# Kernel tuning notes

Measured on AMD Instinct MI355X. Metric: run time of the kernel, lower is better.

The kernel has to match this reference:

```python
import jax, jax.numpy as jnp
import numpy as np

B, T, DIM = 2, 1024, 1024
H, DH, E, K = 8, 64, 5, 3
SCALE = DH ** -0.5


def topk_mask(scores, k):
    # 0/1 mask of the top-k entries along the last (expert) axis
    _, idx = jax.lax.top_k(scores, k)          # [..., k]
    return jax.nn.one_hot(idx, scores.shape[-1], dtype=scores.dtype).sum(-2)


def setup_inputs() -> dict:
    key = jax.random.key(0)
    ks = jax.random.split(key, 7)
    s = DIM ** -0.5
    x = jax.random.normal(ks[0], (B, T, DIM), jnp.float32)
    Wq = jax.random.normal(ks[1], (DIM, H * DH), jnp.float32) * s
    Wk = jax.random.normal(ks[2], (DIM, H * DH), jnp.float32) * s
    Wv = jax.random.normal(ks[3], (DIM, H * E * DH), jnp.float32) * s
    Ws = jax.random.normal(ks[4], (DIM, H * E), jnp.float32) * s
    Wd = jax.random.normal(ks[5], (DIM, H * E), jnp.float32) * s
    # grouped conv weight: per head h, expert e: map dim_head -> dim
    Wo = jax.random.normal(ks[6], (H, E, DIM, DH), jnp.float32) * (DH ** -0.5)
    causal_mask = jnp.triu(jnp.ones((T, T), bool), 1)[None, None]  # [1,1,T,T]
    return {"x": x, "Wq": Wq, "Wk": Wk, "Wv": Wv, "Ws": Ws, "Wd": Wd,
            "Wo": Wo, "causal_mask": causal_mask}


def reference(x, Wq, Wk, Wv, Ws, Wd, Wo, causal_mask):
    # source-side routing scores (soft: gate values kept on top-k)
    ss = jax.nn.sigmoid((x @ Ws).reshape(B, T, H, E))
    ss = ss * topk_mask(ss, K)
    # destination-side routing (hard 0/1 top-k mask)
    sd = topk_mask(jax.nn.sigmoid((x @ Wd).reshape(B, T, H, E)), K)

    q = (x @ Wq).reshape(B, T, H, DH).transpose(0, 2, 1, 3)  # [B,H,T,DH]
    k = (x @ Wk).reshape(B, T, H, DH).transpose(0, 2, 1, 3)
    v_exp = (x @ Wv).reshape(B, T, H, E, DH)                  # per-expert V
    v = jnp.einsum('bthe,bthed->bhtd', ss, v_exp)             # routed V mix

    scores = jnp.einsum('bhid,bhjd->bhij', q * SCALE, k)
    scores = jnp.where(causal_mask, -1e9, scores)
    probs = jax.nn.softmax(scores, axis=-1)
    o = jnp.einsum('bhij,bhjd->bhid', probs, v)               # [B,H,T,DH]

    # expert output projection (h,e: DH -> DIM), gated by sd, summed over h,e
    out = jnp.einsum('bthe,bhtc,hedc->btd', sd, o, Wo)        # [B,T,DIM]
    return out
```

## Files before the change

### kernel.cpp

```cpp
#include <hip/hip_runtime.h>

typedef unsigned short u16;
typedef unsigned long long u64;
typedef __bf16 bf16x8 __attribute__((ext_vector_type(8)));
typedef float floatx4 __attribute__((ext_vector_type(4)));

#define B_   2
#define T_   1024
#define DIM_ 1024
#define H_   8
#define DH_  64
#define E_   5

#define N1   3584
#define M_   2048
#define KOUT 2560

__device__ __forceinline__ u16 f2bf(float f) {
  union { float f; unsigned u; } v; v.f = f;
  unsigned r = v.u + 0x7FFFu + ((v.u >> 16) & 1u);
  return (u16)(r >> 16);
}
__device__ __forceinline__ float bf2f(u16 h) {
  union { unsigned u; float f; } v; v.u = ((unsigned)h) << 16;
  return v.f;
}

__device__ __forceinline__ void async_cp16(const void* g, void* l) {
  __builtin_amdgcn_global_load_lds(
      (const __attribute__((address_space(1))) unsigned int*)g,
      (__attribute__((address_space(3))) unsigned int*)l, 16, 0, 0);
}


__global__ __launch_bounds__(256)
void prep_kernel(const float* __restrict__ Wq, const float* __restrict__ Wk,
                 const float* __restrict__ Wv, const float* __restrict__ Wo,
                 u16* __restrict__ WT, u16* __restrict__ WoT) {
  __shared__ float tile[32][33];
  if (blockIdx.y < 112) {
    int k0 = blockIdx.x * 32;
    int nt = blockIdx.y;
    const float* W; int N, n0, nofs;
    if (nt < 16)      { W = Wq; N = 512;  n0 = nt * 32;        nofs = 0; }
    else if (nt < 32) { W = Wk; N = 512;  n0 = (nt - 16) * 32; nofs = 512; }
    else              { W = Wv; N = 2560; n0 = (nt - 32) * 32; nofs = 1024; }
    int tx = threadIdx.x & 31, ty = threadIdx.x >> 5;
    #pragma unroll
    for (int i = 0; i < 32; i += 8)
      tile[ty + i][tx] = W[(size_t)(k0 + ty + i) * N + n0 + tx];
    __syncthreads();
    #pragma unroll
    for (int i = 0; i < 32; i += 8)
      WT[(size_t)(nofs + n0 + ty + i) * 1024 + k0 + tx] = f2bf(tile[tx][ty + i]);
  } else {
    int id = (blockIdx.y - 112) * 32 + blockIdx.x;
    int i = id * 256 + threadIdx.x;
    int c4 = i & 15;
    int t  = i >> 4;
    int d  = t / 40;
    int he = t - d * 40;
    float4 v = *(const float4*)(Wo + ((size_t)(he * 1024 + d) * 64 + c4 * 4));
    union { u16 s[4]; uint2 u; } o;
    o.s[0] = f2bf(v.x); o.s[1] = f2bf(v.y); o.s[2] = f2bf(v.z); o.s[3] = f2bf(v.w);
    *(uint2*)(WoT + (size_t)d * KOUT + he * 64 + c4 * 4) = o.u;
  }
}


__global__ __launch_bounds__(256)
void logits_kernel(const float* __restrict__ x, const float* __restrict__ Ws,
                   const float* __restrict__ Wd, float* __restrict__ Pl,
                   u16* __restrict__ xb) {
  __shared__ float xs[16][68];
  __shared__ float wt[16][80];
  const int tid = threadIdx.x;
  const int m0 = blockIdx.x * 64;
  const int kbeg = blockIdx.y * 128;
  const int tx = tid & 15, ty = tid >> 4;
  const int srow = tid >> 2, skq = tid & 3;

  float acc[4][5];
  #pragma unroll
  for (int r = 0; r < 4; ++r)
    #pragma unroll
    for (int c = 0; c < 5; ++c) acc[r][c] = 0.f;

  for (int s = 0; s < 8; ++s) {
    const int k0 = kbeg + s * 16;
    __syncthreads();
    {
      float4 v = *(const float4*)(x + (size_t)(m0 + srow) * 1024 + k0 + skq * 4);
      xs[skq * 4 + 0][srow] = v.x; xs[skq * 4 + 1][srow] = v.y;
      xs[skq * 4 + 2][srow] = v.z; xs[skq * 4 + 3][srow] = v.w;
      union { u16 h[4]; uint2 u; } o;
      o.h[0] = f2bf(v.x); o.h[1] = f2bf(v.y); o.h[2] = f2bf(v.z); o.h[3] = f2bf(v.w);
      *(uint2*)(xb + (size_t)(m0 + srow) * 1024 + k0 + skq * 4) = o.u;
    }
    #pragma unroll
    for (int j = 0; j < 5; ++j) {
      int f = j * 256 + tid;
      int kk = f / 80, c = f - kk * 80;
      wt[kk][c] = (c < 40) ? Ws[(size_t)(k0 + kk) * 40 + c]
                           : Wd[(size_t)(k0 + kk) * 40 + c - 40];
    }
    __syncthreads();

    #pragma unroll
    for (int kk = 0; kk < 16; ++kk) {
      float4 xv = *(const float4*)(&xs[kk][ty * 4]);
      float xr[4] = {xv.x, xv.y, xv.z, xv.w};
      #pragma unroll
      for (int c = 0; c < 5; ++c) {
        float wv = wt[kk][tx * 5 + c];
        #pragma unroll
        for (int r = 0; r < 4; ++r) acc[r][c] = fmaf(xr[r], wv, acc[r][c]);
      }
    }
  }

  float* P = Pl + (size_t)blockIdx.y * M_ * 80;
  #pragma unroll
  for (int r = 0; r < 4; ++r)
    #pragma unroll
    for (int c = 0; c < 5; ++c)
      P[(size_t)(m0 + ty * 4 + r) * 80 + tx * 5 + c] = acc[r][c];
}

__global__ __launch_bounds__(256)
void topk_kernel(const float* __restrict__ Pl, float* __restrict__ ssg,
                 u64* __restrict__ sdb) {
  __shared__ float lg[16][80];
  __shared__ unsigned char mb[16][8];
  const int bt0 = blockIdx.x * 16;
  const int tid = threadIdx.x;
  #pragma unroll
  for (int j = 0; j < 5; ++j) {
    int f = j * 256 + tid;
    int r = f / 80, c = f - r * 80;
    float s = 0.f;
    #pragma unroll
    for (int z = 0; z < 8; ++z)
      s += Pl[(size_t)z * M_ * 80 + (size_t)(bt0 + r) * 80 + c];
    lg[r][c] = s;
  }
  __syncthreads();

  const int r = tid >> 4, h = (tid >> 1) & 7, side = tid & 1;
  float z[E_], g[E_]; bool sel[E_];
  #pragma unroll
  for (int e = 0; e < E_; ++e) {
    z[e] = lg[r][side * 40 + h * E_ + e];
    g[e] = 1.f / (1.f + __expf(-z[e]));
    sel[e] = false;
  }
  #pragma unroll
  for (int it = 0; it < 3; ++it) {
    int bi = 0; float bv = -3e38f;
    #pragma unroll
    for (int e = 0; e < E_; ++e)
      if (!sel[e] && z[e] > bv) { bv = z[e]; bi = e; }
    sel[bi] = true;
  }
  if (side == 0) {
    #pragma unroll
    for (int e = 0; e < E_; ++e)
      ssg[(size_t)(bt0 + r) * 40 + h * E_ + e] = sel[e] ? g[e] : 0.f;
  } else {
    unsigned bits = 0;
    #pragma unroll
    for (int e = 0; e < E_; ++e) bits |= (sel[e] ? 1u : 0u) << e;
    mb[r][h] = (unsigned char)bits;
  }
  __syncthreads();
  if (tid < 16) {
    u64 m = 0;
    #pragma unroll
    for (int hh = 0; hh < 8; ++hh) m |= (u64)mb[tid][hh] << (5 * hh);
    sdb[bt0 + tid] = m;
  }
}


__global__ __launch_bounds__(256)
void gemm4w_kernel(const u16* __restrict__ A, const u16* __restrict__ Bm,
                   u16* __restrict__ C, int N, int Kd) {
  constexpr int BK = 32;
  __shared__ __align__(16) u16 As[128 * BK];
  __shared__ __align__(16) u16 Bs[128 * BK];
  const int tid = threadIdx.x;
  const int w = tid >> 6, lane = tid & 63;
  const int ln15 = lane & 15, quad = lane >> 4;
  const int wm = w >> 1, wn = w & 1;
  const int bm0 = blockIdx.x * 128, bn0 = blockIdx.y * 128;
  const int lrow = lane >> 2;
  const int lg8 = (((lane & 3) ^ ((lane >> 3) & 3))) * 8;
  const int swz = (ln15 >> 1) & 3;

  floatx4 acc[4][4];
  #pragma unroll
  for (int i = 0; i < 4; ++i)
    #pragma unroll
    for (int j = 0; j < 4; ++j) acc[i][j] = (floatx4){0.f, 0.f, 0.f, 0.f};

  for (int k0 = 0; k0 < Kd; k0 += BK) {
    __syncthreads();
    #pragma unroll
    for (int j = 0; j < 2; ++j) {
      int i = w * 2 + j;
      async_cp16(A + (size_t)(bm0 + i * 16 + lrow) * Kd + k0 + lg8, (char*)As + i * 1024);
      async_cp16(Bm + (size_t)(bn0 + i * 16 + lrow) * Kd + k0 + lg8, (char*)Bs + i * 1024);
    }
    __builtin_amdgcn_s_waitcnt(0);
    __syncthreads();

    bf16x8 af[4], bf[4];
    #pragma unroll
    for (int mt = 0; mt < 4; ++mt)
      af[mt] = *(const bf16x8*)(As + (wm * 64 + mt * 16 + ln15) * BK + ((quad ^ swz) * 8));
    #pragma unroll
    for (int nt = 0; nt < 4; ++nt)
      bf[nt] = *(const bf16x8*)(Bs + (wn * 64 + nt * 16 + ln15) * BK + ((quad ^ swz) * 8));
    #pragma unroll
    for (int mt = 0; mt < 4; ++mt)
      #pragma unroll
      for (int nt = 0; nt < 4; ++nt)
        acc[mt][nt] = __builtin_amdgcn_mfma_f32_16x16x32_bf16(af[mt], bf[nt], acc[mt][nt], 0, 0, 0);
  }

  #pragma unroll
  for (int mt = 0; mt < 4; ++mt)
    #pragma unroll
    for (int nt = 0; nt < 4; ++nt)
      #pragma unroll
      for (int r = 0; r < 4; ++r) {
        int m = bm0 + wm * 64 + mt * 16 + quad * 4 + r;
        int n = bn0 + wn * 64 + nt * 16 + ln15;
        C[(size_t)m * N + n] = f2bf(acc[mt][nt][r]);
      }
}


__global__ __launch_bounds__(256)
void gemm2f_kernel(const u16* __restrict__ o_bh, const u16* __restrict__ WoT,
                   const u64* __restrict__ sdb, u16* __restrict__ Pk) {
  constexpr int BK = 32, Kd = KOUT;
  __shared__ __align__(16) u16 As[128 * BK];
  __shared__ __align__(16) u16 Bs[128 * BK];
  const int tid = threadIdx.x;
  const int w = tid >> 6, lane = tid & 63;
  const int ln15 = lane & 15, quad = lane >> 4;
  const int wm = w >> 1, wn = w & 1;
  const int bm0 = blockIdx.x * 128, bn0 = blockIdx.y * 128;
  const int b = bm0 >> 10;
  const int t_base = bm0 & 1023;
  const int lrow = lane >> 2;
  const int lg8 = (((lane & 3) ^ ((lane >> 3) & 3))) * 8;
  const int swz = (ln15 >> 1) & 3;
  const int kbeg = blockIdx.z * 640;

  u64 sdr[4];
  #pragma unroll
  for (int mt = 0; mt < 4; ++mt)
    sdr[mt] = sdb[bm0 + wm * 64 + mt * 16 + ln15];

  floatx4 acc[4][4];
  #pragma unroll
  for (int i = 0; i < 4; ++i)
    #pragma unroll
    for (int j = 0; j < 4; ++j) acc[i][j] = (floatx4){0.f, 0.f, 0.f, 0.f};

  for (int k0 = kbeg; k0 < kbeg + 640; k0 += BK) {
    const int he = k0 >> 6;
    const int h = (he * 205) >> 10;
    const int c0 = k0 & 63;
    const u16* abase = o_bh + ((size_t)((b * 8 + h) * 1024 + t_base) * 64) + c0;
    __syncthreads();
    #pragma unroll
    for (int j = 0; j < 2; ++j) {
      int i = w * 2 + j;
      async_cp16(abase + (size_t)(i * 16 + lrow) * 64 + lg8, (char*)As + i * 1024);
      async_cp16(WoT + (size_t)(bn0 + i * 16 + lrow) * Kd + k0 + lg8, (char*)Bs + i * 1024);
    }
    __builtin_amdgcn_s_waitcnt(0);
    __syncthreads();

    bf16x8 af[4], bf[4];
    union { uint4 u; bf16x8 v; } z8; z8.u = (uint4){0u, 0u, 0u, 0u};
    #pragma unroll
    for (int mt = 0; mt < 4; ++mt) {
      af[mt] = *(const bf16x8*)(As + (wm * 64 + mt * 16 + ln15) * BK + ((quad ^ swz) * 8));
      if (!((sdr[mt] >> he) & 1)) af[mt] = z8.v;
    }
    #pragma unroll
    for (int nt = 0; nt < 4; ++nt)
      bf[nt] = *(const bf16x8*)(Bs + (wn * 64 + nt * 16 + ln15) * BK + ((quad ^ swz) * 8));
    #pragma unroll
    for (int mt = 0; mt < 4; ++mt)
      #pragma unroll
      for (int nt = 0; nt < 4; ++nt)
        acc[mt][nt] = __builtin_amdgcn_mfma_f32_16x16x32_bf16(af[mt], bf[nt], acc[mt][nt], 0, 0, 0);
  }

  u16* Cz = Pk + (size_t)blockIdx.z * M_ * 1024;
  #pragma unroll
  for (int mt = 0; mt < 4; ++mt)
    #pragma unroll
    for (int nt = 0; nt < 4; ++nt)
      #pragma unroll
      for (int r = 0; r < 4; ++r) {
        int m = bm0 + wm * 64 + mt * 16 + quad * 4 + r;
        int n = bn0 + wn * 64 + nt * 16 + ln15;
        Cz[(size_t)m * 1024 + n] = f2bf(acc[mt][nt][r]);
      }
}

__global__ void reduce4_kernel(const u16* __restrict__ Pk, float* __restrict__ out) {
  int i = blockIdx.x * 256 + threadIdx.x;
  size_t base = (size_t)i * 8;
  float s[8] = {0.f, 0.f, 0.f, 0.f, 0.f, 0.f, 0.f, 0.f};
  #pragma unroll
  for (int z = 0; z < 4; ++z) {
    union { uint4 v; u16 h[8]; } u;
    u.v = *(const uint4*)(Pk + (size_t)z * M_ * 1024 + base);
    #pragma unroll
    for (int c = 0; c < 8; ++c) s[c] += bf2f(u.h[c]);
  }
  float4 o0 = {s[0], s[1], s[2], s[3]}, o1 = {s[4], s[5], s[6], s[7]};
  *(float4*)(out + base) = o0;
  *(float4*)(out + base + 4) = o1;
}


__global__ __launch_bounds__(256)
void vmix_tr_kernel(const u16* __restrict__ c1, const float* __restrict__ ssg,
                    u16* __restrict__ vT) {
  __shared__ u16 tile[32][33];
  const int bh = blockIdx.x;
  const int b = bh >> 3, h = bh & 7;
  const int t0 = blockIdx.y * 32, d0 = blockIdx.z * 32;
  const int dh = threadIdx.x & 31, tl = threadIdx.x >> 5;
  #pragma unroll
  for (int i = 0; i < 4; ++i) {
    int trow = tl + i * 8;
    size_t bt = (size_t)b * T_ + t0 + trow;
    const u16* ve = c1 + bt * N1 + 1024 + h * (E_ * 64) + d0 + dh;
    const float* g = ssg + bt * 40 + h * E_;
    float s = 0.f;
    #pragma unroll
    for (int e = 0; e < E_; ++e) s = fmaf(g[e], bf2f(ve[e * 64]), s);
    tile[trow][dh] = f2bf(s);
  }
  __syncthreads();
  #pragma unroll
  for (int i = 0; i < 4; ++i) {
    int d = d0 + tl + i * 8;
    vT[((size_t)(b * H_ + h) * DH_ + d) * T_ + t0 + dh] = tile[dh][tl + i * 8];
  }
}


__global__ __launch_bounds__(256)
void attn_kernel(const u16* __restrict__ c1, const u16* __restrict__ vT,
                 u16* __restrict__ o_bh) {
  __shared__ __align__(16) u16 Qs[32 * 64];
  __shared__ __align__(16) u16 Ks[2][64 * 64];
  __shared__ __align__(16) u16 Vs[2][64 * 64];
  __shared__ __align__(16) u16 Ps[2][32 * 72];
  __shared__ float Om[2][32][68];
  __shared__ float Ml[2][32], Ll[2][32];
  const int bx = blockIdx.x;
  const int qi = (bx & 1) ? (bx >> 1) : (31 - (bx >> 1));
  const int bh = blockIdx.y;
  const int b = bh >> 3, h = bh & 7;
  const int tid = threadIdx.x;
  const int w = tid >> 6, lane = tid & 63;
  const int ln15 = lane & 15, quad = lane >> 4;
  const int hh = w >> 1, wq = w & 1;
  const int q0 = qi * 32;
  const int nkt = (qi >> 1) + 1;
  const int h0n = (nkt + 1) >> 1;
  const int r8 = lane >> 3;
  const int g8 = ((lane & 7) ^ ((lane >> 3) & 7)) * 8;
  const int swz = ln15 & 7;

  async_cp16(c1 + (size_t)(b * T_ + q0 + w * 8 + r8) * N1 + h * DH_ + g8,
             (char*)Qs + w * 1024);

  floatx4 O[4];
  float m_st[4], l_st[4];
  #pragma unroll
  for (int j = 0; j < 4; ++j) {
    O[j] = (floatx4){0.f, 0.f, 0.f, 0.f};
    m_st[j] = -3e38f; l_st[j] = 0.f;
  }
  const int qrow = q0 + wq * 16 + quad * 4;

  for (int j = 0; j < h0n; ++j) {
    const int myt = hh ? (h0n + j) : j;
    const bool act = (hh == 0) || (h0n + j < nkt);
    __syncthreads();
    if (w < 2 || h0n + j < nkt) {
      const int tk = (w < 2 ? j : h0n + j) * 64;
      if ((w & 1) == 0) {
        #pragma unroll
        for (int i = 0; i < 8; ++i)
          async_cp16(c1 + (size_t)(b * T_ + tk + i * 8 + r8) * N1 + 512 + h * DH_ + g8,
                     (char*)Ks[w >> 1] + i * 1024);
      } else {
        #pragma unroll
        for (int i = 0; i < 8; ++i)
          async_cp16(vT + (size_t)((b * H_ + h) * DH_ + i * 8 + r8) * T_ + tk + g8,
                     (char*)Vs[w >> 1] + i * 1024);
      }
    }
    __builtin_amdgcn_s_waitcnt(0);
    __syncthreads();

    float p[4][4];
    if (act) {
      const int tk0 = myt * 64;
      floatx4 S[4];
      #pragma unroll
      for (int nt = 0; nt < 4; ++nt) S[nt] = (floatx4){0.f, 0.f, 0.f, 0.f};
      #pragma unroll
      for (int ks = 0; ks < 2; ++ks) {
        bf16x8 a = *(const bf16x8*)(Qs + (wq * 16 + ln15) * 64 + (((ks * 4 + quad) ^ swz)) * 8);
        #pragma unroll
        for (int nt = 0; nt < 4; ++nt) {
          bf16x8 bv = *(const bf16x8*)(&Ks[hh][(nt * 16 + ln15) * 64 + (((ks * 4 + quad) ^ swz)) * 8]);
          S[nt] = __builtin_amdgcn_mfma_f32_16x16x32_bf16(a, bv, S[nt], 0, 0, 0);
        }
      }
      float rmax[4], alpha[4], rsum[4];
      #pragma unroll
      for (int r = 0; r < 4; ++r) rmax[r] = -3e38f;
      #pragma unroll
      for (int nt = 0; nt < 4; ++nt) {
        int col = tk0 + nt * 16 + ln15;
        #pragma unroll
        for (int r = 0; r < 4; ++r) {
          float s = S[nt][r] * 0.125f;
          if (col > qrow + r) s = -3e38f;
          p[nt][r] = s;
          rmax[r] = fmaxf(rmax[r], s);
        }
      }
      #pragma unroll
      for (int r = 0; r < 4; ++r) {
        #pragma unroll
        for (int off = 1; off < 16; off <<= 1)
          rmax[r] = fmaxf(rmax[r], __shfl_xor(rmax[r], off));
        float mn = fmaxf(m_st[r], rmax[r]);
        alpha[r] = __expf(m_st[r] - mn);
        m_st[r] = mn;
        rsum[r] = 0.f;
      }
      #pragma unroll
      for (int nt = 0; nt < 4; ++nt)
        #pragma unroll
        for (int r = 0; r < 4; ++r) {
          float e = __expf(p[nt][r] - m_st[r]);
          p[nt][r] = e;
          rsum[r] += e;
        }
      #pragma unroll
      for (int r = 0; r < 4; ++r) {
        #pragma unroll
        for (int off = 1; off < 16; off <<= 1)
          rsum[r] += __shfl_xor(rsum[r], off);
        l_st[r] = l_st[r] * alpha[r] + rsum[r];
      }
      #pragma unroll
      for (int nt = 0; nt < 4; ++nt)
        #pragma unroll
        for (int r = 0; r < 4; ++r) O[nt][r] *= alpha[r];
      #pragma unroll
      for (int nt = 0; nt < 4; ++nt)
        #pragma unroll
        for (int r = 0; r < 4; ++r)
          Ps[hh][(wq * 16 + quad * 4 + r) * 72 + nt * 16 + ln15] = f2bf(p[nt][r]);
    }
    __syncthreads();
    if (act) {
      #pragma unroll
      for (int ks = 0; ks < 2; ++ks) {
        bf16x8 a = *(const bf16x8*)(&Ps[hh][(wq * 16 + ln15) * 72 + ks * 32 + quad * 8]);
        #pragma unroll
        for (int nt = 0; nt < 4; ++nt) {
          bf16x8 bv = *(const bf16x8*)(&Vs[hh][(nt * 16 + ln15) * 64 + (((ks * 4 + quad) ^ swz)) * 8]);
          O[nt] = __builtin_amdgcn_mfma_f32_16x16x32_bf16(a, bv, O[nt], 0, 0, 0);
        }
      }
    }
  }

  #pragma unroll
  for (int nt = 0; nt < 4; ++nt)
    #pragma unroll
    for (int r = 0; r < 4; ++r)
      Om[hh][wq * 16 + quad * 4 + r][nt * 16 + ln15] = O[nt][r];
  if (ln15 == 0) {
    #pragma unroll
    for (int r = 0; r < 4; ++r) {
      Ml[hh][wq * 16 + quad * 4 + r] = m_st[r];
      Ll[hh][wq * 16 + quad * 4 + r] = l_st[r];
    }
  }
  __syncthreads();

  const int rr = tid >> 3, cg = (tid & 7) * 8;
  float m0 = Ml[0][rr], m1 = Ml[1][rr];
  float l0 = Ll[0][rr], l1 = Ll[1][rr];
  float m = fmaxf(m0, m1);
  float a0 = __expf(m0 - m), a1 = __expf(m1 - m);
  float inv = 1.f / (l0 * a0 + l1 * a1);
  union { u16 s[8]; uint4 v; } o;
  #pragma unroll
  for (int cc = 0; cc < 8; ++cc)
    o.s[cc] = f2bf((Om[0][rr][cg + cc] * a0 + Om[1][rr][cg + cc] * a1) * inv);
  *(uint4*)(o_bh + ((size_t)((b * 8 + h) * 1024 + q0 + rr)) * 64 + cg) = o.v;
}


extern "C" void kernel_launch(void* const* d_in, const int* in_sizes, int n_in,
                              void* d_out, int out_size, void* d_ws, size_t ws_size,
                              hipStream_t stream) {
  const float* x  = (const float*)d_in[0];
  const float* Wq = (const float*)d_in[1];
  const float* Wk = (const float*)d_in[2];
  const float* Wv = (const float*)d_in[3];
  const float* Ws = (const float*)d_in[4];
  const float* Wd = (const float*)d_in[5];
  const float* Wo = (const float*)d_in[6];
  float* out = (float*)d_out;

  char* ws = (char*)d_ws;
  u16*   WoT  = (u16*)(ws + 0);
  u16*   xb   = (u16*)(ws + 5242880);
  u16*   WT   = (u16*)(ws + 9437184);
  u16*   c1   = (u16*)(ws + 16777216);
  float* ssg  = (float*)(ws + 31457280);
  u64*   sdb  = (u64*)(ws + 31784960);
  u16*   o_bh = (u16*)(ws + 31801344);
  u16*   vT   = (u16*)(ws + 33898496);
  u16*   Pk   = (u16*)(ws + 35995648);
  float* Pl   = (float*)(ws + 52772864);

  logits_kernel<<<dim3(32, 8), 256, 0, stream>>>(x, Ws, Wd, Pl, xb);
  topk_kernel<<<128, 256, 0, stream>>>(Pl, ssg, sdb);

  prep_kernel<<<dim3(32, 192), 256, 0, stream>>>(Wq, Wk, Wv, Wo, WT, WoT);

  gemm4w_kernel<<<dim3(16, 28), 256, 0, stream>>>(xb, WT, c1, N1, 1024);

  vmix_tr_kernel<<<dim3(16, 32, 2), 256, 0, stream>>>(c1, ssg, vT);

  attn_kernel<<<dim3(32, 16), 256, 0, stream>>>(c1, vT, o_bh);

  gemm2f_kernel<<<dim3(16, 8, 4), 256, 0, stream>>>(o_bh, WoT, sdb, Pk);
  reduce4_kernel<<<1024, 256, 0, stream>>>(Pk, out);
}
```

Before: 186.9 us.

## Fuse logits, top-k and weight prep into one preamble kernel; widen GEMM BK to 64

Merges the routing-logit GEMV, top-k selection and the weight transpose/convert passes into one launch. Each routing block computes full-K logits for 8 rows using shuffles and LDS reduction, so the partial-logit buffer and its extra kernel disappear. The two bf16 MFMA GEMMs now use a 64-wide K tile with an 8-way XOR swizzle and launch_bounds(256,2), halving the number of barrier/load rounds. In exchange the GEMMs use more LDS per block, and the routing blocks read Ws/Wd straight from global memory without staging them in LDS.

```diff
diff --git a/kernel.cpp b/kernel.cpp
--- a/kernel.cpp
+++ b/kernel.cpp
@@ -32,170 +32,171 @@
       (__attribute__((address_space(3))) unsigned int*)l, 16, 0, 0);
 }
 
+#define XI(r, k) ((r) * 1088 + (k) + (((k) >> 6) << 2))
 
 __global__ __launch_bounds__(256)
-void prep_kernel(const float* __restrict__ Wq, const float* __restrict__ Wk,
-                 const float* __restrict__ Wv, const float* __restrict__ Wo,
-                 u16* __restrict__ WT, u16* __restrict__ WoT) {
-  __shared__ float tile[32][33];
-  if (blockIdx.y < 112) {
-    int k0 = blockIdx.x * 32;
-    int nt = blockIdx.y;
-    const float* W; int N, n0, nofs;
-    if (nt < 16)      { W = Wq; N = 512;  n0 = nt * 32;        nofs = 0; }
-    else if (nt < 32) { W = Wk; N = 512;  n0 = (nt - 16) * 32; nofs = 512; }
-    else              { W = Wv; N = 2560; n0 = (nt - 32) * 32; nofs = 1024; }
-    int tx = threadIdx.x & 31, ty = threadIdx.x >> 5;
-    #pragma unroll
-    for (int i = 0; i < 32; i += 8)
-      tile[ty + i][tx] = W[(size_t)(k0 + ty + i) * N + n0 + tx];
-    __syncthreads();
-    #pragma unroll
-    for (int i = 0; i < 32; i += 8)
-      WT[(size_t)(nofs + n0 + ty + i) * 1024 + k0 + tx] = f2bf(tile[tx][ty + i]);
-  } else {
-    int id = (blockIdx.y - 112) * 32 + blockIdx.x;
-    int i = id * 256 + threadIdx.x;
-    int c4 = i & 15;
-    int t  = i >> 4;
-    int d  = t / 40;
-    int he = t - d * 40;
-    float4 v = *(const float4*)(Wo + ((size_t)(he * 1024 + d) * 64 + c4 * 4));
-    union { u16 s[4]; uint2 u; } o;
-    o.s[0] = f2bf(v.x); o.s[1] = f2bf(v.y); o.s[2] = f2bf(v.z); o.s[3] = f2bf(v.w);
-    *(uint2*)(WoT + (size_t)d * KOUT + he * 64 + c4 * 4) = o.u;
-  }
-}
-
-
-__global__ __launch_bounds__(256)
-void logits_kernel(const float* __restrict__ x, const float* __restrict__ Ws,
-                   const float* __restrict__ Wd, float* __restrict__ Pl,
-                   u16* __restrict__ xb) {
-  __shared__ float xs[16][68];
-  __shared__ float wt[16][80];
+void preamble_kernel(const float* __restrict__ x, const float* __restrict__ Wq,
+                     const float* __restrict__ Wk, const float* __restrict__ Wv,
+                     const float* __restrict__ Ws, const float* __restrict__ Wd,
+                     const float* __restrict__ Wo,
+                     u16* __restrict__ WT, u16* __restrict__ WoT,
+                     float* __restrict__ ssg, u64* __restrict__ sdb,
+                     u16* __restrict__ xb) {
+  __shared__ __align__(16) char smem[47744];
+  const int bx = blockIdx.x;
   const int tid = threadIdx.x;
-  const int m0 = blockIdx.x * 64;
-  const int kbeg = blockIdx.y * 128;
-  const int tx = tid & 15, ty = tid >> 4;
-  const int srow = tid >> 2, skq = tid & 3;
-
-  float acc[4][5];
-  #pragma unroll
-  for (int r = 0; r < 4; ++r)
+
+  if (bx >= 256) {
+    const int pb = bx - 256;
+    const int kx = pb & 31, nt = pb >> 5;
+    if (nt < 112) {
+      float (*tile)[33] = (float(*)[33])smem;
+      int k0 = kx * 32;
+      const float* W; int N, n0, nofs;
+      if (nt < 16)      { W = Wq; N = 512;  n0 = nt * 32;        nofs = 0; }
+      else if (nt < 32) { W = Wk; N = 512;  n0 = (nt - 16) * 32; nofs = 512; }
+      else              { W = Wv; N = 2560; n0 = (nt - 32) * 32; nofs = 1024; }
+      int tx = tid & 31, ty = tid >> 5;
+      #pragma unroll
+      for (int i = 0; i < 32; i += 8)
+        tile[ty + i][tx] = W[(size_t)(k0 + ty + i) * N + n0 + tx];
+      __syncthreads();
+      #pragma unroll
+      for (int i = 0; i < 32; i += 8)
+        WT[(size_t)(nofs + n0 + ty + i) * 1024 + k0 + tx] = f2bf(tile[tx][ty + i]);
+    } else {
+      int id = (nt - 112) * 32 + kx;
+      int i = id * 256 + tid;
+      int c4 = i & 15;
+      int t  = i >> 4;
+      int d  = t / 40;
+      int he = t - d * 40;
+      float4 v = *(const float4*)(Wo + ((size_t)(he * 1024 + d) * 64 + c4 * 4));
+      union { u16 s[4]; uint2 u; } o;
+      o.s[0] = f2bf(v.x); o.s[1] = f2bf(v.y); o.s[2] = f2bf(v.z); o.s[3] = f2bf(v.w);
+      *(uint2*)(WoT + (size_t)d * KOUT + he * 64 + c4 * 4) = o.u;
+    }
+    return;
+  }
+
+  float* xs = (float*)smem;
+  float* ps = xs + 8 * 1088;
+  float* lg = ps + 4 * 640;
+  unsigned char* mb = (unsigned char*)(lg + 640);
+  const int bt0 = bx * 8;
+
+  for (int i = tid; i < 2048; i += 256) {
+    int r = i >> 8, j = i & 255;
+    float4 v = ((const float4*)(x + (size_t)(bt0 + r) * 1024))[j];
+    *(float4*)(xs + XI(r, j * 4)) = v;
+    union { u16 h[4]; uint2 u; } o;
+    o.h[0] = f2bf(v.x); o.h[1] = f2bf(v.y); o.h[2] = f2bf(v.z); o.h[3] = f2bf(v.w);
+    *(uint2*)(xb + (size_t)(bt0 + r) * 1024 + j * 4) = o.u;
+  }
+  __syncthreads();
+
+  const int cx = tid & 15;
+  const int ky = tid >> 4;
+  float acc[8][5];
+  #pragma unroll
+  for (int r = 0; r < 8; ++r)
     #pragma unroll
     for (int c = 0; c < 5; ++c) acc[r][c] = 0.f;
 
-  for (int s = 0; s < 8; ++s) {
-    const int k0 = kbeg + s * 16;
-    __syncthreads();
-    {
-      float4 v = *(const float4*)(x + (size_t)(m0 + srow) * 1024 + k0 + skq * 4);
-      xs[skq * 4 + 0][srow] = v.x; xs[skq * 4 + 1][srow] = v.y;
-      xs[skq * 4 + 2][srow] = v.z; xs[skq * 4 + 3][srow] = v.w;
-      union { u16 h[4]; uint2 u; } o;
-      o.h[0] = f2bf(v.x); o.h[1] = f2bf(v.y); o.h[2] = f2bf(v.z); o.h[3] = f2bf(v.w);
-      *(uint2*)(xb + (size_t)(m0 + srow) * 1024 + k0 + skq * 4) = o.u;
-    }
-    #pragma unroll
-    for (int j = 0; j < 5; ++j) {
-      int f = j * 256 + tid;
-      int kk = f / 80, c = f - kk * 80;
-      wt[kk][c] = (c < 40) ? Ws[(size_t)(k0 + kk) * 40 + c]
-                           : Wd[(size_t)(k0 + kk) * 40 + c - 40];
-    }
-    __syncthreads();
-
-    #pragma unroll
-    for (int kk = 0; kk < 16; ++kk) {
-      float4 xv = *(const float4*)(&xs[kk][ty * 4]);
-      float xr[4] = {xv.x, xv.y, xv.z, xv.w};
-      #pragma unroll
-      for (int c = 0; c < 5; ++c) {
-        float wv = wt[kk][tx * 5 + c];
-        #pragma unroll
-        for (int r = 0; r < 4; ++r) acc[r][c] = fmaf(xr[r], wv, acc[r][c]);
-      }
-    }
-  }
-
-  float* P = Pl + (size_t)blockIdx.y * M_ * 80;
-  #pragma unroll
-  for (int r = 0; r < 4; ++r)
-    #pragma unroll
-    for (int c = 0; c < 5; ++c)
-      P[(size_t)(m0 + ty * 4 + r) * 80 + tx * 5 + c] = acc[r][c];
-}
-
-__global__ __launch_bounds__(256)
-void topk_kernel(const float* __restrict__ Pl, float* __restrict__ ssg,
-                 u64* __restrict__ sdb) {
-  __shared__ float lg[16][80];
-  __shared__ unsigned char mb[16][8];
-  const int bt0 = blockIdx.x * 16;
-  const int tid = threadIdx.x;
-  #pragma unroll
-  for (int j = 0; j < 5; ++j) {
-    int f = j * 256 + tid;
-    int r = f / 80, c = f - r * 80;
-    float s = 0.f;
-    #pragma unroll
-    for (int z = 0; z < 8; ++z)
-      s += Pl[(size_t)z * M_ * 80 + (size_t)(bt0 + r) * 80 + c];
-    lg[r][c] = s;
+  for (int q4 = 0; q4 < 16; ++q4) {
+    const int k = ky * 64 + q4 * 4;
+    float4 xr[8];
+    #pragma unroll
+    for (int r = 0; r < 8; ++r) xr[r] = *(const float4*)(xs + XI(r, k));
+    #pragma unroll
+    for (int c = 0; c < 5; ++c) {
+      const int col = cx * 5 + c;
+      const float* Wp = (col < 40) ? (Ws + col) : (Wd + col - 40);
+      float w0 = Wp[(size_t)(k + 0) * 40], w1 = Wp[(size_t)(k + 1) * 40];
+      float w2 = Wp[(size_t)(k + 2) * 40], w3 = Wp[(size_t)(k + 3) * 40];
+      #pragma unroll
+      for (int r = 0; r < 8; ++r) {
+        float a = acc[r][c];
+        a = fmaf(xr[r].x, w0, a); a = fmaf(xr[r].y, w1, a);
+        a = fmaf(xr[r].z, w2, a); a = fmaf(xr[r].w, w3, a);
+        acc[r][c] = a;
+      }
+    }
+  }
+
+  #pragma unroll
+  for (int r = 0; r < 8; ++r)
+    #pragma unroll
+    for (int c = 0; c < 5; ++c) {
+      float a = acc[r][c];
+      a += __shfl_xor(a, 16);
+      a += __shfl_xor(a, 32);
+      acc[r][c] = a;
+    }
+  const int w = tid >> 6, lane = tid & 63;
+  if (lane < 16) {
+    #pragma unroll
+    for (int r = 0; r < 8; ++r)
+      #pragma unroll
+      for (int c = 0; c < 5; ++c)
+        ps[w * 640 + r * 80 + lane * 5 + c] = acc[r][c];
   }
   __syncthreads();
-
-  const int r = tid >> 4, h = (tid >> 1) & 7, side = tid & 1;
-  float z[E_], g[E_]; bool sel[E_];
-  #pragma unroll
-  for (int e = 0; e < E_; ++e) {
-    z[e] = lg[r][side * 40 + h * E_ + e];
-    g[e] = 1.f / (1.f + __expf(-z[e]));
-    sel[e] = false;
-  }
-  #pragma unroll
-  for (int it = 0; it < 3; ++it) {
-    int bi = 0; float bv = -3e38f;
-    #pragma unroll
-    for (int e = 0; e < E_; ++e)
-      if (!sel[e] && z[e] > bv) { bv = z[e]; bi = e; }
-    sel[bi] = true;
-  }
-  if (side == 0) {
-    #pragma unroll
-    for (int e = 0; e < E_; ++e)
-      ssg[(size_t)(bt0 + r) * 40 + h * E_ + e] = sel[e] ? g[e] : 0.f;
-  } else {
-    unsigned bits = 0;
-    #pragma unroll
-    for (int e = 0; e < E_; ++e) bits |= (sel[e] ? 1u : 0u) << e;
-    mb[r][h] = (unsigned char)bits;
-  }
+  for (int idx = tid; idx < 640; idx += 256)
+    lg[idx] = ps[idx] + ps[640 + idx] + ps[1280 + idx] + ps[1920 + idx];
   __syncthreads();
-  if (tid < 16) {
+
+  if (tid < 128) {
+    const int r = tid >> 4, h = (tid >> 1) & 7, side = tid & 1;
+    float z[E_], g[E_]; bool sel[E_];
+    #pragma unroll
+    for (int e = 0; e < E_; ++e) {
+      z[e] = lg[r * 80 + side * 40 + h * E_ + e];
+      g[e] = 1.f / (1.f + __expf(-z[e]));
+      sel[e] = false;
+    }
+    #pragma unroll
+    for (int it = 0; it < 3; ++it) {
+      int bi = 0; float bv = -3e38f;
+      #pragma unroll
+      for (int e = 0; e < E_; ++e)
+        if (!sel[e] && z[e] > bv) { bv = z[e]; bi = e; }
+      sel[bi] = true;
+    }
+    if (side == 0) {
+      #pragma unroll
+      for (int e = 0; e < E_; ++e)
+        ssg[(size_t)(bt0 + r) * 40 + h * E_ + e] = sel[e] ? g[e] : 0.f;
+    } else {
+      unsigned bits = 0;
+      #pragma unroll
+      for (int e = 0; e < E_; ++e) bits |= (sel[e] ? 1u : 0u) << e;
+      mb[r * 8 + h] = (unsigned char)bits;
+    }
+  }
+  __syncthreads();
+  if (tid < 8) {
     u64 m = 0;
     #pragma unroll
-    for (int hh = 0; hh < 8; ++hh) m |= (u64)mb[tid][hh] << (5 * hh);
+    for (int hh = 0; hh < 8; ++hh) m |= (u64)mb[tid * 8 + hh] << (5 * hh);
     sdb[bt0 + tid] = m;
   }
 }
 
 
-__global__ __launch_bounds__(256)
+__global__ __launch_bounds__(256, 2)
 void gemm4w_kernel(const u16* __restrict__ A, const u16* __restrict__ Bm,
                    u16* __restrict__ C, int N, int Kd) {
-  constexpr int BK = 32;
-  __shared__ __align__(16) u16 As[128 * BK];
-  __shared__ __align__(16) u16 Bs[128 * BK];
+  __shared__ __align__(16) u16 As[128 * 64];
+  __shared__ __align__(16) u16 Bs[128 * 64];
   const int tid = threadIdx.x;
   const int w = tid >> 6, lane = tid & 63;
   const int ln15 = lane & 15, quad = lane >> 4;
   const int wm = w >> 1, wn = w & 1;
   const int bm0 = blockIdx.x * 128, bn0 = blockIdx.y * 128;
-  const int lrow = lane >> 2;
-  const int lg8 = (((lane & 3) ^ ((lane >> 3) & 3))) * 8;
-  const int swz = (ln15 >> 1) & 3;
+  const int r8 = lane >> 3;
+  const int g8 = ((lane & 7) ^ r8) * 8;
+  const int swz = ln15 & 7;
 
   floatx4 acc[4][4];
   #pragma unroll
@@ -203,29 +204,32 @@
     #pragma unroll
     for (int j = 0; j < 4; ++j) acc[i][j] = (floatx4){0.f, 0.f, 0.f, 0.f};
 
-  for (int k0 = 0; k0 < Kd; k0 += BK) {
-    __syncthreads();
-    #pragma unroll
-    for (int j = 0; j < 2; ++j) {
-      int i = w * 2 + j;
-      async_cp16(A + (size_t)(bm0 + i * 16 + lrow) * Kd + k0 + lg8, (char*)As + i * 1024);
-      async_cp16(Bm + (size_t)(bn0 + i * 16 + lrow) * Kd + k0 + lg8, (char*)Bs + i * 1024);
+  for (int k0 = 0; k0 < Kd; k0 += 64) {
+    __syncthreads();
+    #pragma unroll
+    for (int j = 0; j < 4; ++j) {
+      int i = w * 4 + j;
+      async_cp16(A + (size_t)(bm0 + i * 8 + r8) * Kd + k0 + g8, (char*)As + i * 1024);
+      async_cp16(Bm + (size_t)(bn0 + i * 8 + r8) * Kd + k0 + g8, (char*)Bs + i * 1024);
     }
     __builtin_amdgcn_s_waitcnt(0);
     __syncthreads();
 
-    bf16x8 af[4], bf[4];
-    #pragma unroll
-    for (int mt = 0; mt < 4; ++mt)
-      af[mt] = *(const bf16x8*)(As + (wm * 64 + mt * 16 + ln15) * BK + ((quad ^ swz) * 8));
-    #pragma unroll
-    for (int nt = 0; nt < 4; ++nt)
-      bf[nt] = *(const bf16x8*)(Bs + (wn * 64 + nt * 16 + ln15) * BK + ((quad ^ swz) * 8));
-    #pragma unroll
-    for (int mt = 0; mt < 4; ++mt)
+    #pragma unroll
+    for (int t = 0; t < 2; ++t) {
+      bf16x8 af[4], bf[4];
+      #pragma unroll
+      for (int mt = 0; mt < 4; ++mt)
+        af[mt] = *(const bf16x8*)(As + (wm * 64 + mt * 16 + ln15) * 64 + (((t * 4 + quad) ^ swz) * 8));
       #pragma unroll
       for (int nt = 0; nt < 4; ++nt)
-        acc[mt][nt] = __builtin_amdgcn_mfma_f32_16x16x32_bf16(af[mt], bf[nt], acc[mt][nt], 0, 0, 0);
+        bf[nt] = *(const bf16x8*)(Bs + (wn * 64 + nt * 16 + ln15) * 64 + (((t * 4 + quad) ^ swz) * 8));
+      #pragma unroll
+      for (int mt = 0; mt < 4; ++mt)
+        #pragma unroll
+        for (int nt = 0; nt < 4; ++nt)
+          acc[mt][nt] = __builtin_amdgcn_mfma_f32_16x16x32_bf16(af[mt], bf[nt], acc[mt][nt], 0, 0, 0);
+    }
   }
 
   #pragma unroll
@@ -241,12 +245,11 @@
 }
 
 
-__global__ __launch_bounds__(256)
+__global__ __launch_bounds__(256, 2)
 void gemm2f_kernel(const u16* __restrict__ o_bh, const u16* __restrict__ WoT,
                    const u64* __restrict__ sdb, u16* __restrict__ Pk) {
-  constexpr int BK = 32, Kd = KOUT;
-  __shared__ __align__(16) u16 As[128 * BK];
-  __shared__ __align__(16) u16 Bs[128 * BK];
+  __shared__ __align__(16) u16 As[128 * 64];
+  __shared__ __align__(16) u16 Bs[128 * 64];
   const int tid = threadIdx.x;
   const int w = tid >> 6, lane = tid & 63;
   const int ln15 = lane & 15, quad = lane >> 4;
@@ -254,9 +257,9 @@
   const int bm0 = blockIdx.x * 128, bn0 = blockIdx.y * 128;
   const int b = bm0 >> 10;
   const int t_base = bm0 & 1023;
-  const int lrow = lane >> 2;
-  const int lg8 = (((lane & 3) ^ ((lane >> 3) & 3))) * 8;
-  const int swz = (ln15 >> 1) & 3;
+  const int r8 = lane >> 3;
+  const int g8 = ((lane & 7) ^ r8) * 8;
+  const int swz = ln15 & 7;
   const int kbeg = blockIdx.z * 640;
 
   u64 sdr[4];
@@ -270,36 +273,38 @@
     #pragma unroll
     for (int j = 0; j < 4; ++j) acc[i][j] = (floatx4){0.f, 0.f, 0.f, 0.f};
 
-  for (int k0 = kbeg; k0 < kbeg + 640; k0 += BK) {
+  for (int k0 = kbeg; k0 < kbeg + 640; k0 += 64) {
     const int he = k0 >> 6;
     const int h = (he * 205) >> 10;
-    const int c0 = k0 & 63;
-    const u16* abase = o_bh + ((size_t)((b * 8 + h) * 1024 + t_base) * 64) + c0;
-    __syncthreads();
-    #pragma unroll
-    for (int j = 0; j < 2; ++j) {
-      int i = w * 2 + j;
-      async_cp16(abase + (size_t)(i * 16 + lrow) * 64 + lg8, (char*)As + i * 1024);
-      async_cp16(WoT + (size_t)(bn0 + i * 16 + lrow) * Kd + k0 + lg8, (char*)Bs + i * 1024);
+    const u16* abase = o_bh + (size_t)((b * 8 + h) * 1024 + t_base) * 64;
+    __syncthreads();
+    #pragma unroll
+    for (int j = 0; j < 4; ++j) {
+      int i = w * 4 + j;
+      async_cp16(abase + (size_t)(i * 8 + r8) * 64 + g8, (char*)As + i * 1024);
+      async_cp16(WoT + (size_t)(bn0 + i * 8 + r8) * KOUT + k0 + g8, (char*)Bs + i * 1024);
     }
     __builtin_amdgcn_s_waitcnt(0);
     __syncthreads();
 
-    bf16x8 af[4], bf[4];
     union { uint4 u; bf16x8 v; } z8; z8.u = (uint4){0u, 0u, 0u, 0u};
     #pragma unroll
-    for (int mt = 0; mt < 4; ++mt) {
-      af[mt] = *(const bf16x8*)(As + (wm * 64 + mt * 16 + ln15) * BK + ((quad ^ swz) * 8));
-      if (!((sdr[mt] >> he) & 1)) af[mt] = z8.v;
-    }
-    #pragma unroll
-    for (int nt = 0; nt < 4; ++nt)
-      bf[nt] = *(const bf16x8*)(Bs + (wn * 64 + nt * 16 + ln15) * BK + ((quad ^ swz) * 8));
-    #pragma unroll
-    for (int mt = 0; mt < 4; ++mt)
+    for (int t = 0; t < 2; ++t) {
+      bf16x8 af[4], bf[4];
+      #pragma unroll
+      for (int mt = 0; mt < 4; ++mt) {
+        af[mt] = *(const bf16x8*)(As + (wm * 64 + mt * 16 + ln15) * 64 + (((t * 4 + quad) ^ swz) * 8));
+        if (!((sdr[mt] >> he) & 1)) af[mt] = z8.v;
+      }
       #pragma unroll
       for (int nt = 0; nt < 4; ++nt)
-        acc[mt][nt] = __builtin_amdgcn_mfma_f32_16x16x32_bf16(af[mt], bf[nt], acc[mt][nt], 0, 0, 0);
+        bf[nt] = *(const bf16x8*)(Bs + (wn * 64 + nt * 16 + ln15) * 64 + (((t * 4 + quad) ^ swz) * 8));
+      #pragma unroll
+      for (int mt = 0; mt < 4; ++mt)
+        #pragma unroll
+        for (int nt = 0; nt < 4; ++nt)
+          acc[mt][nt] = __builtin_amdgcn_mfma_f32_16x16x32_bf16(af[mt], bf[nt], acc[mt][nt], 0, 0, 0);
+    }
   }
 
   u16* Cz = Pk + (size_t)blockIdx.z * M_ * 1024;
@@ -545,12 +550,9 @@
   u16*   o_bh = (u16*)(ws + 31801344);
   u16*   vT   = (u16*)(ws + 33898496);
   u16*   Pk   = (u16*)(ws + 35995648);
-  float* Pl   = (float*)(ws + 52772864);
-
-  logits_kernel<<<dim3(32, 8), 256, 0, stream>>>(x, Ws, Wd, Pl, xb);
-  topk_kernel<<<128, 256, 0, stream>>>(Pl, ssg, sdb);
-
-  prep_kernel<<<dim3(32, 192), 256, 0, stream>>>(Wq, Wk, Wv, Wo, WT, WoT);
+
+  preamble_kernel<<<6400, 256, 0, stream>>>(x, Wq, Wk, Wv, Ws, Wd, Wo,
+                                            WT, WoT, ssg, sdb, xb);
 
   gemm4w_kernel<<<dim3(16, 28), 256, 0, stream>>>(xb, WT, c1, N1, 1024);
 
```

Result: faster. 179.0 us (-4.2%).
